# Performance work log

Hardware: AMD Instinct MI355X
Metric: run time of the kernel (lower is better)

The kernel has to match this reference:

```python
import jax, jax.numpy as jnp
import numpy as np

HIDDEN = 1024
BATCH, SEQ = 4, 2048

def setup_inputs() -> dict:
    key = jax.random.key(0)
    kx, kq, kk, kv, ko = jax.random.split(key, 5)
    s = 1.0 / np.sqrt(HIDDEN)
    return {
        "x": jax.random.normal(kx, (BATCH, SEQ, HIDDEN), dtype=jnp.float32),
        "Wq": jax.random.normal(kq, (HIDDEN, HIDDEN), dtype=jnp.float32) * s,
        "Wk": jax.random.normal(kk, (HIDDEN, HIDDEN), dtype=jnp.float32) * s,
        "Wv": jax.random.normal(kv, (HIDDEN, HIDDEN), dtype=jnp.float32) * s,
        "Wo": jax.random.normal(ko, (HIDDEN, HIDDEN), dtype=jnp.float32) * s,
    }

def reference(x, Wq, Wk, Wv, Wo):
    # torch Linear: y = x @ W.T; weights here stored as [out, in]
    q = jnp.einsum('bsd,ed->bse', x, Wq)
    k = jnp.einsum('bsd,ed->bse', x, Wk)
    v = jnp.einsum('bsd,ed->bse', x, Wv)
    score = jnp.einsum('bqe,bke->bqk', q, k)  # unscaled, per source
    score = jax.nn.softmax(score, axis=-1)
    out = jnp.einsum('bqk,bke->bqe', score, v)
    return jnp.einsum('bse,fe->bsf', out, Wo)
```

## Files before the change

### kernel.cpp

```cpp
#include <hip/hip_runtime.h>
#include <stdint.h>


typedef _Float16 f16_t;
typedef _Float16 f16x8 __attribute__((ext_vector_type(8)));
typedef _Float16 f16x4 __attribute__((ext_vector_type(4)));
typedef float    f32x4 __attribute__((ext_vector_type(4)));
typedef uint32_t u32;

__device__ __forceinline__ void gld_lds16(const void* g, void* l) {
    __builtin_amdgcn_global_load_lds(
        (const __attribute__((address_space(1))) void*)g,
        (__attribute__((address_space(3))) void*)l, 16, 0, 0);
}

__device__ __forceinline__ f16x8 ld128(const void* p) {
    f16x8 r;
    const u32 a = (u32)(uintptr_t)(__attribute__((address_space(3))) const void*)p;
    asm volatile("ds_read_b128 %0, %1" : "=v"(r) : "v"(a));
    return r;
}

template<int EPI>
__global__ __launch_bounds__(512, 1)
void gemm256(const f16_t* __restrict__ A0, const f16_t* __restrict__ A1,
             const f16_t* __restrict__ A2,
             const f16_t* __restrict__ B0, const f16_t* __restrict__ B1,
             const f16_t* __restrict__ B2,
             int NK, int lda, int ldb, long sA, long sB, long sC,
             void* __restrict__ C0v, int ldc,
             int nbx, int plane)
{
    __shared__ __align__(1024) char smem[131072];

    const int nwg = (int)gridDim.x;
    int id = (int)blockIdx.x;
    id = (id & 7) * (nwg >> 3) + (id >> 3);
    const int bz  = id / plane;
    const int rem = id - bz * plane;
    const int by  = rem / nbx;
    const int bx  = rem - by * nbx;
    const long bm = (long)by * 256;
    const long bn = (long)bx * 256;
    const long zA = (long)bz * sA, zB = (long)bz * sB;

    const int tid  = threadIdx.x;
    const int lane = tid & 63;
    const int wid  = tid >> 6;
    const int wr   = wid >> 2;
    const int wc   = wid & 3;
    const int fr   = lane & 15;
    const int kg   = lane >> 4;

    const int srow = tid >> 3;
    const int scol = ((tid & 7) ^ ((tid >> 4) & 7)) << 3;
    const int ldsw = wid << 10;

    const int swzb    = (fr & 14) << 3;
    const int koff[2] = { (kg * 16) ^ swzb, (64 + kg * 16) ^ swzb };
    const int aBase   = wr * 16384 + fr * 128;
    const int bBase   = 32768 + (wc >> 1) * 16384 + (wc & 1) * 8192 + fr * 128;

    f32x4 acc[8][4] = {};
    f16x8 bfr[4][2];

    auto stage = [&](int kt, int part, int buf) {
        const int seg    = kt >> 4;
        const int klocal = (kt & 15) << 6;
        const bool isB = part < 2;
        const f16_t* base;
        if (isB) base = (seg == 0) ? B0 : (seg == 1 ? B1 : B2);
        else     base = (seg == 0) ? A0 : (seg == 1 ? A1 : A2);
        const long rowb = (isB ? (bn + part * 128) : (bm + (part - 2) * 128)) + srow;
        const long zoff = isB ? zB : zA;
        const int  ld   = isB ? ldb : lda;
        const int  poff = isB ? (32768 + part * 16384) : ((part - 2) * 16384);
        #pragma unroll
        for (int c = 0; c < 2; ++c) {
            const f16_t* g = base + zoff + (rowb + c * 64) * (long)ld + klocal + scol;
            gld_lds16(g, smem + buf * 65536 + poff + c * 8192 + ldsw);
        }
    };

    #pragma unroll
    for (int ht = 0; ht < 7; ++ht) stage(ht >> 2, ht & 3, (ht >> 2) & 1);
    asm volatile("s_waitcnt vmcnt(6)" ::: "memory");
    __builtin_amdgcn_s_barrier();

    const int NI = NK >> 1;
    #pragma unroll 1
    for (int i = 0; i < NI; ++i) {
        const bool last = (i == NI - 1);
        #pragma unroll
        for (int p = 0; p < 8; ++p) {
            const int q  = p & 3;
            const int cb = (p >> 2) * 65536;
            if (q == 0) {
                #pragma unroll
                for (int fn = 0; fn < 4; ++fn)
                    #pragma unroll
                    for (int kh = 0; kh < 2; ++kh)
                        bfr[fn][kh] = ld128(smem + cb + bBase
                                            + fn * 2048 + koff[kh]);
            }
            f16x8 afr[2][2];
            #pragma unroll
            for (int m2 = 0; m2 < 2; ++m2)
                #pragma unroll
                for (int kh = 0; kh < 2; ++kh)
                    afr[m2][kh] = ld128(smem + cb + aBase
                                        + (q * 2 + m2) * 2048 + koff[kh]);
            const int sc = (7 + p) >> 2;
            if (p == 0 || !last) stage(2 * i + sc, (7 + p) & 3, sc & 1);
            __builtin_amdgcn_s_barrier();
            asm volatile("s_waitcnt lgkmcnt(0)" ::: "memory");
            __builtin_amdgcn_sched_barrier(0);
            __builtin_amdgcn_s_setprio(1);
            #pragma unroll
            for (int m2 = 0; m2 < 2; ++m2)
                #pragma unroll
                for (int fn = 0; fn < 4; ++fn)
                    #pragma unroll
                    for (int kh = 0; kh < 2; ++kh)
                        acc[q * 2 + m2][fn] = __builtin_amdgcn_mfma_f32_16x16x32_f16(
                            afr[m2][kh], bfr[fn][kh], acc[q * 2 + m2][fn], 0, 0, 0);
            __builtin_amdgcn_s_setprio(0);
            if (q == 3) {
                if (last) asm volatile("s_waitcnt vmcnt(0)" ::: "memory");
                else      asm volatile("s_waitcnt vmcnt(6)" ::: "memory");
            }
            __builtin_amdgcn_s_barrier();
        }
    }

    const int rq = kg * 4;
    #pragma unroll
    for (int m = 0; m < 8; ++m) {
        #pragma unroll
        for (int fn = 0; fn < 4; ++fn) {
            const long col = bn + wc * 64 + fn * 16 + fr;
            #pragma unroll
            for (int r = 0; r < 4; ++r) {
                const long row = bm + wr * 128 + m * 16 + rq + r;
                const float v = acc[m][fn][r];
                if constexpr (EPI == 0) {
                    ((float*)C0v)[(long)bz * sC + row * ldc + col] = v;
                } else {
                    const long off = (col >= 1024)
                        ? 8388608L + row * 1024 + (col - 1024)
                        : row * 1024 + col;
                    ((f16_t*)C0v)[off] = (f16_t)v;
                }
            }
        }
    }
}

#define BM 128
#define BN 128
#define BK 32

template<int EPI>
__global__ __launch_bounds__(256, 2)
void gemm_nt(const f16_t* __restrict__ A, const f16_t* __restrict__ B,
             int K, int lda, int ldb, long sA, long sB, long sC,
             void* __restrict__ C0v, int ldc, int nbx, int nby)
{
    __shared__ f16_t As[BM * BK];
    __shared__ f16_t Bs[BN * BK];

    const int nwg = (int)gridDim.x;
    int id = (int)blockIdx.x;
    id = (id & 7) * (nwg >> 3) + (id >> 3);
    const int plane = nbx * nby;
    const int bz  = id / plane;
    const int rem = id - bz * plane;
    const int by  = rem / nbx;
    const int bx  = rem - by * nbx;

    const long bm = (long)by * BM;
    const long bn = (long)bx * BN;

    const f16_t* A0 = A + (long)bz * sA;
    const f16_t* B0 = B + (long)bz * sB;

    const int tid  = threadIdx.x;
    const int lane = tid & 63;
    const int wid  = tid >> 6;
    const int wr   = wid >> 1;
    const int wc   = wid & 1;

    const int srow = tid >> 2;
    const int sgc  = (((tid & 3) ^ ((tid >> 3) & 3)) << 3);
    const int ldsb = wid * 512;

    const int fr  = lane & 15;
    const int kgs = (((lane >> 4) ^ ((lane >> 1) & 3)) << 3);

    f32x4 acc[4][4] = {};

    const long arow = (bm + srow) * (long)lda;
    const long brow = (bn + srow) * (long)ldb;

    for (int k0 = 0; k0 < K; k0 += BK) {
        const f16_t* a = A0 + arow + k0 + sgc;
        const f16_t* b = B0 + brow + k0 + sgc;
        gld_lds16(a,             &As[ldsb]);
        gld_lds16(a + 64L * lda, &As[2048 + ldsb]);
        gld_lds16(b,             &Bs[ldsb]);
        gld_lds16(b + 64L * ldb, &Bs[2048 + ldsb]);
        __syncthreads();

        f16x8 af[4], bg[4];
        #pragma unroll
        for (int m = 0; m < 4; ++m)
            af[m] = *(const f16x8*)&As[(wr * 64 + m * 16 + fr) * BK + kgs];
        #pragma unroll
        for (int n = 0; n < 4; ++n)
            bg[n] = *(const f16x8*)&Bs[(wc * 64 + n * 16 + fr) * BK + kgs];
        #pragma unroll
        for (int m = 0; m < 4; ++m)
            #pragma unroll
            for (int n = 0; n < 4; ++n)
                acc[m][n] = __builtin_amdgcn_mfma_f32_16x16x32_f16(
                    af[m], bg[n], acc[m][n], 0, 0, 0);
        __syncthreads();
    }

    const int rq = (lane >> 4) * 4;
    #pragma unroll
    for (int m = 0; m < 4; ++m) {
        #pragma unroll
        for (int n = 0; n < 4; ++n) {
            const long col = bn + wc * 64 + n * 16 + fr;
            #pragma unroll
            for (int r = 0; r < 4; ++r) {
                const long row = bm + wr * 64 + m * 16 + rq + r;
                const long idx = (long)bz * sC + row * ldc + col;
                const float v = acc[m][n][r];
                if constexpr (EPI == 0) ((float*)C0v)[idx] = v;
                else                    ((f16_t*)C0v)[idx] = (f16_t)v;
            }
        }
    }
}

__global__ __launch_bounds__(256)
void prep(const float* __restrict__ x,  const float* __restrict__ Wq,
          const float* __restrict__ Wk, const float* __restrict__ Wo,
          const float* __restrict__ Wv,
          f16_t* __restrict__ xh, f16_t* __restrict__ xl,
          f16_t* __restrict__ wqk, f16_t* __restrict__ wo16,
          f16_t* __restrict__ wvT)
{
    const int bid = blockIdx.x;
    const int tid = threadIdx.x;
    if (bid < 4096) {
        const int i = (bid * 256 + tid) * 8;
        const f32x4 v0 = *(const f32x4*)&x[i];
        const f32x4 v1 = *(const f32x4*)&x[i + 4];
        f16x8 h, l;
        #pragma unroll
        for (int j = 0; j < 4; ++j) {
            h[j]     = (f16_t)v0[j];
            l[j]     = (f16_t)(v0[j] - (float)h[j]);
            h[j + 4] = (f16_t)v1[j];
            l[j + 4] = (f16_t)(v1[j] - (float)h[j + 4]);
        }
        *(f16x8*)&xh[i] = h;
        *(f16x8*)&xl[i] = l;
    } else if (bid < 5632) {
        const float* src; f16_t* dst;
        if      (bid < 4608) { src = Wq; dst = wqk;               }
        else if (bid < 5120) { src = Wk; dst = wqk + 1024 * 1024; }
        else                 { src = Wo; dst = wo16;              }
        const int lb = (bid < 4608) ? bid - 4096 : (bid < 5120 ? bid - 4608 : bid - 5120);
        const int i = (lb * 256 + tid) * 8;
        const f32x4 v0 = *(const f32x4*)&src[i];
        const f32x4 v1 = *(const f32x4*)&src[i + 4];
        f16x8 h;
        #pragma unroll
        for (int j = 0; j < 4; ++j) {
            h[j]     = (f16_t)v0[j];
            h[j + 4] = (f16_t)v1[j];
        }
        *(f16x8*)&dst[i] = h;
    } else {
        __shared__ float tile[64][65];
        const int b  = bid - 5632;
        const int br = b >> 4, bc = b & 15;
        const int c  = tid & 63;
        #pragma unroll
        for (int j = 0; j < 16; ++j) {
            const int r = j * 4 + (tid >> 6);
            tile[r][c] = Wv[(br * 64 + r) * 1024 + bc * 64 + c];
        }
        __syncthreads();
        #pragma unroll
        for (int j = 0; j < 16; ++j) {
            const int r = j * 4 + (tid >> 6);
            wvT[(bc * 64 + r) * 1024 + br * 64 + c] = (f16_t)tile[c][r];
        }
    }
}

__global__ __launch_bounds__(256)
void softmax_rows(const float* __restrict__ Sc, f16_t* __restrict__ P)
{
    constexpr int NC = 2048;
    const int row = blockIdx.x;
    const int tid = threadIdx.x;
    const float* s = Sc + (size_t)row * NC;

    float v[8];
    *(f32x4*)&v[0] = *(const f32x4*)&s[tid * 8];
    *(f32x4*)&v[4] = *(const f32x4*)&s[tid * 8 + 4];

    float m = v[0];
    #pragma unroll
    for (int j = 1; j < 8; ++j) m = fmaxf(m, v[j]);
    #pragma unroll
    for (int off = 1; off < 64; off <<= 1) m = fmaxf(m, __shfl_xor(m, off));

    __shared__ float redm[4], reds[4];
    if ((tid & 63) == 0) redm[tid >> 6] = m;
    __syncthreads();
    m = fmaxf(fmaxf(redm[0], redm[1]), fmaxf(redm[2], redm[3]));

    float sum = 0.f;
    #pragma unroll
    for (int j = 0; j < 8; ++j) { v[j] = __expf(v[j] - m); sum += v[j]; }
    #pragma unroll
    for (int off = 1; off < 64; off <<= 1) sum += __shfl_xor(sum, off);
    if ((tid & 63) == 0) reds[tid >> 6] = sum;
    __syncthreads();
    sum = reds[0] + reds[1] + reds[2] + reds[3];

    const float inv = 1.0f / sum;
    f16x8 o;
    #pragma unroll
    for (int j = 0; j < 8; ++j) o[j] = (f16_t)(v[j] * inv);
    *(f16x8*)(P + (size_t)row * NC + tid * 8) = o;
}

extern "C" void kernel_launch(void* const* d_in, const int* in_sizes, int n_in,
                              void* d_out, int out_size, void* d_ws, size_t ws_size,
                              hipStream_t stream)
{
    const float* x  = (const float*)d_in[0];
    const float* Wq = (const float*)d_in[1];
    const float* Wk = (const float*)d_in[2];
    const float* Wv = (const float*)d_in[3];
    const float* Wo = (const float*)d_in[4];
    float* out = (float*)d_out;

    constexpr long H = 1024, S = 2048, B = 4, NT = B * S;

    char* ws = (char*)d_ws;
    const size_t MB = 1u << 20;
    f16_t* xh    = (f16_t*)(ws + 0);
    float* score = (float*)(ws + 0);
    f16_t* wqk   = (f16_t*)(ws + 64 * MB);
    f16_t* wo16  = (f16_t*)(ws + 68 * MB);
    f16_t* wvT   = (f16_t*)(ws + 70 * MB);
    f16_t* wvo   = (f16_t*)(ws + 72 * MB);
    f16_t* qh    = (f16_t*)(ws + 80 * MB);
    f16_t* kh    = (f16_t*)(ws + 96 * MB);
    f16_t* P     = (f16_t*)(ws + 80 * MB);
    f16_t* uT    = (f16_t*)(ws + 112 * MB);
    f16_t* xl    = (f16_t*)(ws + 128 * MB);

    prep<<<dim3(5888), dim3(256), 0, stream>>>(x, Wq, Wk, Wo, Wv,
                                               xh, xl, wqk, wo16, wvT);

    gemm256<3><<<dim3(256), dim3(512), 0, stream>>>(
        xh, xl, xh, wqk, wqk, wqk, 32, (int)H, (int)H, 0L, 0L, 0L,
        qh, (int)H, 8, 256);

    gemm_nt<1><<<dim3(64), dim3(256), 0, stream>>>(
        wo16, wvT, (int)H, (int)H, (int)H, 0L, 0L, 0L, wvo, (int)H, 8, 8);

    gemm_nt<1><<<dim3(512), dim3(256), 0, stream>>>(
        wvo, xh, (int)H, (int)H, (int)H, 0L, 0L, 0L, uT, (int)NT, 64, 8);

    gemm256<0><<<dim3(256), dim3(512), 0, stream>>>(
        qh, qh, qh, kh, kh, kh, 16, (int)H, (int)H,
        S * H, S * H, S * S, score, (int)S, 8, 64);

    softmax_rows<<<dim3(B * S), dim3(256), 0, stream>>>(score, P);

    gemm_nt<0><<<dim3(512), dim3(256), 0, stream>>>(
        P, uT, (int)S, (int)S, (int)NT, S * S, S, S * H, out, (int)H, 8, 16);
}
```

Measured before the change: 236.4 us.

## Add pipelined 128x256 MFMA GEMM kernel for value projection and output GEMMs

Adds a new 512-thread GEMM kernel with 128x256 output tiles, BK=64, double-buffered direct global-to-LDS loads with XOR swizzling, and staged prefetch interleaved across the four inner sub-steps. It replaces the 128x128 gemm_nt for both the uT projection and the P·uT output GEMM. The intent is more operand reuse per tile and overlap of global loads with the MFMA work. In exchange the kernel uses 96KB of LDS at one block per CU, and the grid drops to 256 blocks, which reduces occupancy.

```diff
diff --git a/kernel.cpp b/kernel.cpp
--- a/kernel.cpp
+++ b/kernel.cpp
@@ -151,6 +151,121 @@
                         : row * 1024 + col;
                     ((f16_t*)C0v)[off] = (f16_t)v;
                 }
+            }
+        }
+    }
+}
+
+template<int EPI>
+__global__ __launch_bounds__(512, 1)
+void gemm128x256(const f16_t* __restrict__ A, const f16_t* __restrict__ B,
+                 int NK, int lda, int ldb, long sA, long sB, long sC,
+                 void* __restrict__ C0v, int ldc, int nbx, int plane)
+{
+    __shared__ __align__(1024) char smem[98304];
+
+    const int nwg = (int)gridDim.x;
+    int id = (int)blockIdx.x;
+    id = (id & 7) * (nwg >> 3) + (id >> 3);
+    const int bz  = id / plane;
+    const int rem = id - bz * plane;
+    const int by  = rem / nbx;
+    const int bx  = rem - by * nbx;
+    const long bm = (long)by * 128;
+    const long bn = (long)bx * 256;
+    const f16_t* Ab = A + (long)bz * sA;
+    const f16_t* Bb = B + (long)bz * sB;
+
+    const int tid  = threadIdx.x;
+    const int lane = tid & 63;
+    const int wid  = tid >> 6;
+    const int wr   = wid >> 2;
+    const int wc   = wid & 3;
+    const int fr   = lane & 15;
+    const int kg   = lane >> 4;
+
+    const int srow = tid >> 3;
+    const int scol = ((tid & 7) ^ ((tid >> 4) & 7)) << 3;
+    const int ldsw = wid << 10;
+
+    const int swzb    = (fr & 14) << 3;
+    const int koff[2] = { (kg * 16) ^ swzb, (64 + kg * 16) ^ swzb };
+    const int aBase   = wr * 8192 + fr * 128;
+    const int bBase   = 16384 + wc * 8192 + fr * 128;
+
+    f32x4 acc[4][4] = {};
+    f16x8 bfr[4][2];
+
+    auto stage = [&](int kt, int part, int buf) {
+        const bool isB = part < 2;
+        const f16_t* base = isB ? Bb : Ab;
+        const long rowb = (isB ? (bn + part * 128) : bm) + srow;
+        const int  ld   = isB ? ldb : lda;
+        const int  poff = isB ? (16384 + part * 16384) : 0;
+        #pragma unroll
+        for (int c = 0; c < 2; ++c) {
+            const f16_t* g = base + (rowb + c * 64) * (long)ld + kt * 64 + scol;
+            gld_lds16(g, smem + buf * 49152 + poff + c * 8192 + ldsw);
+        }
+    };
+
+    stage(0, 0, 0); stage(0, 1, 0); stage(0, 2, 0);
+    stage(1, 0, 1); stage(1, 1, 1);
+    asm volatile("s_waitcnt vmcnt(4)" ::: "memory");
+    __builtin_amdgcn_s_barrier();
+
+    #pragma unroll 1
+    for (int T = 0; T < NK; ++T) {
+        const int cb = (T & 1) * 49152;
+        #pragma unroll
+        for (int q = 0; q < 4; ++q) {
+            if (q == 0) {
+                #pragma unroll
+                for (int fn = 0; fn < 4; ++fn)
+                    #pragma unroll
+                    for (int kh = 0; kh < 2; ++kh)
+                        bfr[fn][kh] = ld128(smem + cb + bBase
+                                            + fn * 2048 + koff[kh]);
+            }
+            f16x8 afr[2];
+            #pragma unroll
+            for (int kh = 0; kh < 2; ++kh)
+                afr[kh] = ld128(smem + cb + aBase + q * 2048 + koff[kh]);
+            if (q == 0 && T + 1 < NK) stage(T + 1, 2, (T + 1) & 1);
+            if (q == 1 && T + 2 < NK) stage(T + 2, 0, T & 1);
+            if (q == 2 && T + 2 < NK) stage(T + 2, 1, T & 1);
+            __builtin_amdgcn_s_barrier();
+            asm volatile("s_waitcnt lgkmcnt(0)" ::: "memory");
+            __builtin_amdgcn_sched_barrier(0);
+            __builtin_amdgcn_s_setprio(1);
+            #pragma unroll
+            for (int fn = 0; fn < 4; ++fn)
+                #pragma unroll
+                for (int kh = 0; kh < 2; ++kh)
+                    acc[q][fn] = __builtin_amdgcn_mfma_f32_16x16x32_f16(
+                        afr[kh], bfr[fn][kh], acc[q][fn], 0, 0, 0);
+            __builtin_amdgcn_s_setprio(0);
+            if (q == 3) {
+                if (T >= NK - 2) asm volatile("s_waitcnt vmcnt(0)" ::: "memory");
+                else             asm volatile("s_waitcnt vmcnt(4)" ::: "memory");
+            }
+            __builtin_amdgcn_s_barrier();
+        }
+    }
+
+    const int rq = kg * 4;
+    #pragma unroll
+    for (int q = 0; q < 4; ++q) {
+        #pragma unroll
+        for (int fn = 0; fn < 4; ++fn) {
+            const long col = bn + wc * 64 + fn * 16 + fr;
+            #pragma unroll
+            for (int r = 0; r < 4; ++r) {
+                const long row = bm + wr * 64 + q * 16 + rq + r;
+                const long idx = (long)bz * sC + row * ldc + col;
+                const float v = acc[q][fn][r];
+                if constexpr (EPI == 0) ((float*)C0v)[idx] = v;
+                else                    ((f16_t*)C0v)[idx] = (f16_t)v;
             }
         }
     }
@@ -380,8 +495,8 @@
     gemm_nt<1><<<dim3(64), dim3(256), 0, stream>>>(
         wo16, wvT, (int)H, (int)H, (int)H, 0L, 0L, 0L, wvo, (int)H, 8, 8);
 
-    gemm_nt<1><<<dim3(512), dim3(256), 0, stream>>>(
-        wvo, xh, (int)H, (int)H, (int)H, 0L, 0L, 0L, uT, (int)NT, 64, 8);
+    gemm128x256<1><<<dim3(256), dim3(512), 0, stream>>>(
+        wvo, xh, 16, (int)H, (int)H, 0L, 0L, 0L, uT, (int)NT, 32, 256);
 
     gemm256<0><<<dim3(256), dim3(512), 0, stream>>>(
         qh, qh, qh, kh, kh, kh, 16, (int)H, (int)H,
@@ -389,6 +504,6 @@
 
     softmax_rows<<<dim3(B * S), dim3(256), 0, stream>>>(score, P);
 
-    gemm_nt<0><<<dim3(512), dim3(256), 0, stream>>>(
-        P, uT, (int)S, (int)S, (int)NT, S * S, S, S * H, out, (int)H, 8, 16);
-}
+    gemm128x256<0><<<dim3(256), dim3(512), 0, stream>>>(
+        P, uT, 32, (int)S, (int)NT, S * S, S, S * H, out, (int)H, 4, 64);
+}
```

After: 228.8 us. -3.2%, faster.
